# Performance work log

Measured on AMD Instinct MI355X. Metric: run time of the kernel, lower is better.

## Reference

```python
import jax, jax.numpy as jnp
import numpy as np
import math

B, I, C = 64, 512, 32
PRED, PL, ST, NH = 96, 16, 8, 8
WKS = (24, 168, 336)
PN = (I + ST - PL) // ST + 1  # 64 patches (padding_patch='end')

def _gelu(x):
    return jax.nn.gelu(x, approximate=False)  # torch nn.GELU default (erf)

def _ln(x, g, b, eps=1e-5):
    m = x.mean(-1, keepdims=True)
    v = ((x - m) ** 2).mean(-1, keepdims=True)
    return (x - m) / jnp.sqrt(v + eps) * g + b

def setup_inputs() -> dict:
    keys = jax.random.split(jax.random.key(0), 64)
    ki = iter(keys)
    def nrm(sh, sc=0.02):
        return (jax.random.normal(next(ki), sh) * sc).astype(jnp.float32)
    inp = {}
    inp['s'] = jax.random.normal(next(ki), (B, I, C), jnp.float32)
    inp['t'] = jax.random.normal(next(ki), (B, I, C), jnp.float32)
    inp['cycle_index'] = jax.random.randint(next(ki), (B,), 0, 336)
    # router: Linear(C, C//2) -> GELU -> Linear(C//2, num_scales)
    inp['rw1'] = nrm((C // 2, C)); inp['rb1'] = jnp.zeros(C // 2)
    inp['rw2'] = nrm((3, C // 2)); inp['rb2'] = jnp.zeros(3)
    # per-scale amplitude / phase tables (Wk, C)
    inp['A0'] = nrm((WKS[0], C), 1.0); inp['A1'] = nrm((WKS[1], C), 1.0); inp['A2'] = nrm((WKS[2], C), 1.0)
    inp['P0'] = (jax.random.uniform(next(ki), (WKS[0], C)) * 2 * math.pi).astype(jnp.float32)
    inp['P1'] = (jax.random.uniform(next(ki), (WKS[1], C)) * 2 * math.pi).astype(jnp.float32)
    inp['P2'] = (jax.random.uniform(next(ki), (WKS[2], C)) * 2 * math.pi).astype(jnp.float32)
    # PB_RPA (phase-biased relative patch attention), n_embd=PL, n_head=NH
    inp['Wqkv'] = nrm((3 * PL, PL)); inp['bqkv'] = jnp.zeros(3 * PL)
    inp['Wo'] = nrm((PL, PL)); inp['bo'] = jnp.zeros(PL)
    inp['alpha'] = jnp.ones(())
    # bn2 over channel dim = patch_num
    inp['bn_g'] = jnp.ones(PN); inp['bn_b'] = jnp.zeros(PN)
    inp['W3'] = nrm((2 * PRED, PN * PL)); inp['b3'] = jnp.zeros(2 * PRED)
    inp['W4'] = nrm((PRED, 2 * PRED)); inp['b4'] = jnp.zeros(PRED)
    inp['W5'] = nrm((4 * PRED, I)); inp['b5'] = jnp.zeros(4 * PRED)
    inp['W6'] = nrm((PRED, 2 * PRED)); inp['b6'] = jnp.zeros(PRED)
    inp['W7'] = nrm((PRED, PRED // 2)); inp['b7'] = jnp.zeros(PRED)
    inp['W8'] = nrm((PRED, 2 * PRED)); inp['b8'] = jnp.zeros(PRED)
    inp['ln1_g'] = jnp.ones(2 * PRED); inp['ln1_b'] = jnp.zeros(2 * PRED)
    inp['ln2_g'] = jnp.ones(PRED // 2); inp['ln2_b'] = jnp.zeros(PRED // 2)
    # TrendEnhancer: Conv1d(C, C, 3, pad=1) gated residual
    inp['te_w'] = nrm((C, C, 3)); inp['te_b'] = jnp.zeros(C)
    return inp

def _forward(s, t, cycle_index, rw1, rb1, rw2, rb2, A0, A1, A2, P0, P1, P2,
             Wqkv, bqkv, Wo, bo, alpha, bn_g, bn_b, W3, b3, W4, b4, W5, b5,
             W6, b6, W7, b7, W8, b8, ln1_g, ln1_b, ln2_g, ln2_b, te_w, te_b):
    s = s.transpose(0, 2, 1)  # (B,C,I)
    t = t.transpose(0, 2, 1)
    # router -> per-scale softmax weights (B, num_scales)
    h = _gelu(s.mean(-1) @ rw1.T + rb1)
    p = jax.nn.softmax(h @ rw2.T + rb2, axis=-1)
    ar = jnp.arange(I)
    cs, ps = [], []
    for Atab, Ptab, Wk in ((A0, P0, WKS[0]), (A1, P1, WKS[1]), (A2, P2, WKS[2])):
        idx = (cycle_index[:, None] + ar) % Wk            # (B,I) data-dependent gather
        A = jax.nn.softplus(Atab[idx]).transpose(0, 2, 1)  # (B,C,I)
        phi = Ptab[idx].transpose(0, 2, 1)
        Qr = A * jnp.cos(phi)                              # Qi=A*sin(phi) is unused in hermitian_attn
        S = jnp.einsum('bcl,bck->blk', Qr, s) / math.sqrt(C)
        Aw = jax.nn.softmax(S, axis=-1)
        cs.append(jnp.einsum('blk,bck->bcl', Aw, s))
        ps.append(phi)
    c_stack = jnp.stack(cs, 1)    # (B,3,C,I)
    phi_stack = jnp.stack(ps, 1)
    beta = p[:, :, None, None]
    s = s + (beta * c_stack).sum(1)
    fused_phi = (beta * phi_stack).sum(1)  # (B,C,I)
    N = B * C
    s = s.reshape(N, I)
    t = t.reshape(N, I)
    phi = jnp.repeat(fused_phi.mean(1), C, axis=0)  # (N,I)
    # padding_patch='end' -> replicate-pad last `stride` steps
    s = jnp.concatenate([s, jnp.repeat(s[:, -1:], ST, 1)], 1)
    phi = jnp.concatenate([phi, jnp.repeat(phi[:, -1:], ST, 1)], 1)
    widx = jnp.arange(PN)[:, None] * ST + jnp.arange(PL)
    sp = s[:, widx]                # (N, PN, PL) unfold
    phis = phi[:, widx].mean(-1)   # (N, PN)
    # PB_RPA: MHA over patches with phase-difference bias
    qkv = sp @ Wqkv.T + bqkv
    q, k, v = jnp.split(qkv, 3, axis=-1)
    hd = PL // NH
    def heads(x):
        return x.reshape(N, PN, NH, hd).transpose(0, 2, 1, 3)
    q, k, v = heads(q), heads(k), heads(v)
    bias = alpha * jnp.cos(phis[:, None, :, None] - phis[:, None, None, :])  # (N,1,PN,PN)
    sc = jnp.einsum('nhtd,nhsd->nhts', q, k) / math.sqrt(hd) + bias
    Aw = jax.nn.softmax(sc, axis=-1)
    o = jnp.einsum('nhts,nhsd->nhtd', Aw, v).transpose(0, 2, 1, 3).reshape(N, PN, PL)
    o = o @ Wo.T + bo
    sx = _gelu(sp + o)
    # bn2: BatchNorm1d over channel=patch_num (training-mode batch stats)
    mu = sx.mean((0, 2), keepdims=True)
    var = ((sx - mu) ** 2).mean((0, 2), keepdims=True)
    sx = (sx - mu) / jnp.sqrt(var + 1e-5) * bn_g[None, :, None] + bn_b[None, :, None]
    sx = sx.reshape(N, PN * PL)
    sx = _gelu(sx @ W3.T + b3) @ W4.T + b4  # (N, PRED)
    # trend branch
    u = t @ W5.T + b5                       # (N, 4*PRED)
    u = u.reshape(N, 2 * PRED, 2).mean(-1)  # AvgPool1d(2)
    u = _ln(u, ln1_g, ln1_b)
    u = u @ W6.T + b6
    u = u.reshape(N, PRED // 2, 2).mean(-1)
    u = _ln(u, ln2_g, ln2_b)
    u = u @ W7.T + b7                       # (N, PRED)
    u = u.reshape(B, C, PRED)
    f = jnp.fft.rfft(u, axis=-1)
    mask = (jnp.arange(f.shape[-1]) < 5).astype(f.dtype)
    u = u + jnp.fft.irfft(f * mask, n=PRED, axis=-1)
    y = jax.lax.conv_general_dilated(u, te_w, (1,), [(1, 1)],
                                     dimension_numbers=('NCH', 'OIH', 'NCH')) + te_b[None, :, None]
    u = (u + _gelu(y)).reshape(N, PRED)     # TrendEnhancer gated-conv residual
    x = jnp.concatenate([sx, u], 1) @ W8.T + b8
    return x.reshape(B, C, PRED).transpose(0, 2, 1)  # (B, pred_len, C)

def reference(s, t, cycle_index, rw1, rb1, rw2, rb2, A0, A1, A2, P0, P1, P2,
              Wqkv, bqkv, Wo, bo, alpha, bn_g, bn_b, W3, b3, W4, b4, W5, b5,
              W6, b6, W7, b7, W8, b8, ln1_g, ln1_b, ln2_g, ln2_b, te_w, te_b):
    return _forward(s, t, cycle_index, rw1, rb1, rw2, rb2, A0, A1, A2, P0, P1, P2,
                    Wqkv, bqkv, Wo, bo, alpha, bn_g, bn_b, W3, b3, W4, b4, W5, b5,
                    W6, b6, W7, b7, W8, b8, ln1_g, ln1_b, ln2_g, ln2_b, te_w, te_b)
```

## Files before the change

kernel.cpp:

```cpp
#include <hip/hip_runtime.h>
#include <math.h>

#define B_    64
#define I_    512
#define C_    32
#define PRED_ 96
#define PL_   16
#define ST_   8
#define NH_   8
#define PN_   64
#define N_    2048

typedef short bf16x8 __attribute__((ext_vector_type(8)));
typedef float f32x4 __attribute__((ext_vector_type(4)));
typedef bf16x8 __attribute__((may_alias)) bf16x8_a;
typedef uint2 __attribute__((may_alias)) uint2_a;
typedef uint4 __attribute__((may_alias)) uint4_a;

__device__ __forceinline__ float geluf(float x) {
    return 0.5f * x * (1.0f + erff(x * 0.70710678118654752f));
}
__device__ __forceinline__ float softplusf(float x) {
    return fmaxf(x, 0.0f) + log1pf(__expf(-fabsf(x)));
}
__device__ __forceinline__ unsigned short f2bf(float x) {
    union { float f; unsigned int u; } v; v.f = x;
    unsigned int r = v.u + 0x7fffu + ((v.u >> 16) & 1u);
    return (unsigned short)(r >> 16);
}

__global__ void k_headphi(const float* __restrict__ s, const float* __restrict__ rw1,
                          const float* __restrict__ rb1, const float* __restrict__ rw2,
                          const float* __restrict__ rb2,
                          const float* __restrict__ P0, const float* __restrict__ P1,
                          const float* __restrict__ P2, const int* __restrict__ cyc,
                          float* __restrict__ wp, float* __restrict__ phis) {
    int b = blockIdx.x, t = threadIdx.x;
    __shared__ float part[8][32];
    __shared__ float smean[32];
    __shared__ float h[16];
    __shared__ float wpl[3];
    __shared__ float pm[I_];
    int c = t & 31, chunk = t >> 5;
    float acc = 0.f;
    for (int l = chunk * 64; l < chunk * 64 + 64; ++l)
        acc += s[((size_t)b * I_ + l) * C_ + c];
    part[chunk][c] = acc;
    __syncthreads();
    if (t < 32) {
        float v = 0.f;
#pragma unroll
        for (int i = 0; i < 8; ++i) v += part[i][t];
        smean[t] = v * (1.0f / I_);
    }
    __syncthreads();
    if (t < 16) {
        float a = rb1[t];
#pragma unroll
        for (int c2 = 0; c2 < 32; ++c2) a += smean[c2] * rw1[t * 32 + c2];
        h[t] = geluf(a);
    }
    __syncthreads();
    if (t == 0) {
        float lg[3], mx = -1e30f;
        for (int k = 0; k < 3; ++k) {
            float a = rb2[k];
            for (int j = 0; j < 16; ++j) a += h[j] * rw2[k * 16 + j];
            lg[k] = a; mx = fmaxf(mx, a);
        }
        float d = 0.f;
        for (int k = 0; k < 3; ++k) { lg[k] = __expf(lg[k] - mx); d += lg[k]; }
        float inv = 1.f / d;
        for (int k = 0; k < 3; ++k) { wpl[k] = lg[k] * inv; wp[b * 3 + k] = lg[k] * inv; }
    }
    __syncthreads();
    float p0 = wpl[0], p1 = wpl[1], p2 = wpl[2];
    int cy = cyc[b];
    for (int l = t; l < I_; l += 256) {
        float acc2 = 0.f;
        {
            int idx = (cy + l) % 24;
            const float4* r = (const float4*)(P0 + idx * 32);
            float s4 = 0.f;
#pragma unroll
            for (int i = 0; i < 8; ++i) { float4 v = r[i]; s4 += v.x + v.y + v.z + v.w; }
            acc2 += p0 * s4;
        }
        {
            int idx = (cy + l) % 168;
            const float4* r = (const float4*)(P1 + idx * 32);
            float s4 = 0.f;
#pragma unroll
            for (int i = 0; i < 8; ++i) { float4 v = r[i]; s4 += v.x + v.y + v.z + v.w; }
            acc2 += p1 * s4;
        }
        {
            int idx = (cy + l) % 336;
            const float4* r = (const float4*)(P2 + idx * 32);
            float s4 = 0.f;
#pragma unroll
            for (int i = 0; i < 8; ++i) { float4 v = r[i]; s4 += v.x + v.y + v.z + v.w; }
            acc2 += p2 * s4;
        }
        pm[l] = acc2 * (1.0f / 32.0f);
    }
    __syncthreads();
    if (t < PN_) {
        float sum = 0.f;
#pragma unroll
        for (int j = 0; j < 16; ++j) {
            int l = t * ST_ + j; if (l > 511) l = 511;
            sum += pm[l];
        }
        phis[b * PN_ + t] = sum * (1.0f / 16.0f);
    }
}

__global__ void __launch_bounds__(512) k_attn_mfma(
        const float* __restrict__ s, const int* __restrict__ cyc,
        const float* __restrict__ A0, const float* __restrict__ A1, const float* __restrict__ A2,
        const float* __restrict__ P0, const float* __restrict__ P1, const float* __restrict__ P2,
        const float* __restrict__ wp, float* __restrict__ pcs) {
    int k3 = blockIdx.x, b = blockIdx.y;
    int t = threadIdx.x;
    int wid = t >> 6, lane = t & 63;
    int l15 = lane & 15, lg = lane >> 4;

    __shared__ unsigned short s_lds[512][40];
    __shared__ unsigned short sT[32][520];
    __shared__ unsigned short Pt[8][64][40];

    {
        int row = t;
        const float4* src = (const float4*)(s + ((size_t)b * I_ + row) * C_);
        unsigned short bv[32];
#pragma unroll
        for (int i = 0; i < 8; ++i) {
            float4 v = src[i];
            bv[4 * i + 0] = f2bf(v.x); bv[4 * i + 1] = f2bf(v.y);
            bv[4 * i + 2] = f2bf(v.z); bv[4 * i + 3] = f2bf(v.w);
        }
#pragma unroll
        for (int i = 0; i < 4; ++i) {
            uint4 pk;
            pk.x = (unsigned)bv[8 * i + 0] | ((unsigned)bv[8 * i + 1] << 16);
            pk.y = (unsigned)bv[8 * i + 2] | ((unsigned)bv[8 * i + 3] << 16);
            pk.z = (unsigned)bv[8 * i + 4] | ((unsigned)bv[8 * i + 5] << 16);
            pk.w = (unsigned)bv[8 * i + 6] | ((unsigned)bv[8 * i + 7] << 16);
            *((uint4_a*)&s_lds[row][8 * i]) = pk;
        }
#pragma unroll
        for (int cc = 0; cc < 32; ++cc) sT[cc][row] = bv[cc];
    }

    const float* Atab; const float* Ptab; int Wk;
    if (k3 == 0)      { Atab = A0; Ptab = P0; Wk = 24;  }
    else if (k3 == 1) { Atab = A1; Ptab = P1; Wk = 168; }
    else              { Atab = A2; Ptab = P2; Wk = 336; }
    float wpv = wp[b * 3 + k3];
    int cy = cyc[b];
    bf16x8 qrf[4];
#pragma unroll
    for (int qt = 0; qt < 4; ++qt) {
        int q = wid * 64 + qt * 16 + l15;
        int idx = (cy + q) % Wk;
        const float4* Ar = (const float4*)(Atab + idx * 32 + lg * 8);
        const float4* Pr = (const float4*)(Ptab + idx * 32 + lg * 8);
        float4 a0 = Ar[0], a1 = Ar[1], p0 = Pr[0], p1 = Pr[1];
        float qv[8];
        qv[0] = softplusf(a0.x) * __cosf(p0.x);
        qv[1] = softplusf(a0.y) * __cosf(p0.y);
        qv[2] = softplusf(a0.z) * __cosf(p0.z);
        qv[3] = softplusf(a0.w) * __cosf(p0.w);
        qv[4] = softplusf(a1.x) * __cosf(p1.x);
        qv[5] = softplusf(a1.y) * __cosf(p1.y);
        qv[6] = softplusf(a1.z) * __cosf(p1.z);
        qv[7] = softplusf(a1.w) * __cosf(p1.w);
        bf16x8 f;
#pragma unroll
        for (int j = 0; j < 8; ++j) f[j] = (short)f2bf(qv[j]);
        qrf[qt] = f;
    }
    __syncthreads();

    const float rs = 0.17677669529663687f;
    f32x4 acc[4][2];
#pragma unroll
    for (int qt = 0; qt < 4; ++qt)
#pragma unroll
        for (int ct = 0; ct < 2; ++ct) acc[qt][ct] = (f32x4){0.f, 0.f, 0.f, 0.f};
    float dacc[4] = {0.f, 0.f, 0.f, 0.f};

    for (int kc = 0; kc < 16; ++kc) {
        int key0 = kc * 32;
        bf16x8 a0 = *((const bf16x8_a*)&s_lds[key0 + l15][lg * 8]);
        bf16x8 a1 = *((const bf16x8_a*)&s_lds[key0 + 16 + l15][lg * 8]);
        f32x4 stv[4][2];
#pragma unroll
        for (int qt = 0; qt < 4; ++qt) {
            stv[qt][0] = __builtin_amdgcn_mfma_f32_16x16x32_bf16(a0, qrf[qt], (f32x4){0.f,0.f,0.f,0.f}, 0, 0, 0);
            stv[qt][1] = __builtin_amdgcn_mfma_f32_16x16x32_bf16(a1, qrf[qt], (f32x4){0.f,0.f,0.f,0.f}, 0, 0, 0);
        }
#pragma unroll
        for (int qt = 0; qt < 4; ++qt) {
#pragma unroll
            for (int h = 0; h < 2; ++h) {
                unsigned short pb[4];
                float ds = 0.f;
#pragma unroll
                for (int r = 0; r < 4; ++r) {
                    float e = __expf(stv[qt][h][r] * rs);
                    unsigned short ub = f2bf(e);
                    pb[r] = ub;
                    union { unsigned int u; float f; } bb; bb.u = ((unsigned int)ub) << 16;
                    ds += bb.f;
                }
                dacc[qt] += ds;
                uint2 w2;
                w2.x = (unsigned)pb[0] | ((unsigned)pb[1] << 16);
                w2.y = (unsigned)pb[2] | ((unsigned)pb[3] << 16);
                *((uint2_a*)&Pt[wid][qt * 16 + l15][h * 16 + lg * 4]) = w2;
            }
        }
        bf16x8 b0 = *((const bf16x8_a*)&sT[l15][key0 + lg * 8]);
        bf16x8 b1 = *((const bf16x8_a*)&sT[16 + l15][key0 + lg * 8]);
#pragma unroll
        for (int qt = 0; qt < 4; ++qt) {
            bf16x8 pa = *((const bf16x8_a*)&Pt[wid][qt * 16 + l15][lg * 8]);
            acc[qt][0] = __builtin_amdgcn_mfma_f32_16x16x32_bf16(pa, b0, acc[qt][0], 0, 0, 0);
            acc[qt][1] = __builtin_amdgcn_mfma_f32_16x16x32_bf16(pa, b1, acc[qt][1], 0, 0, 0);
        }
    }

#pragma unroll
    for (int qt = 0; qt < 4; ++qt) {
        float dq = dacc[qt];
        dq += __shfl_xor(dq, 16);
        dq += __shfl_xor(dq, 32);
        float invd[4];
#pragma unroll
        for (int r = 0; r < 4; ++r) {
            float dr = __shfl(dq, 4 * lg + r);
            invd[r] = wpv / dr;
        }
        int qbase = wid * 64 + qt * 16 + 4 * lg;
#pragma unroll
        for (int ct = 0; ct < 2; ++ct) {
            int c = ct * 16 + l15;
            float4 o;
            o.x = acc[qt][ct][0] * invd[0];
            o.y = acc[qt][ct][1] * invd[1];
            o.z = acc[qt][ct][2] * invd[2];
            o.w = acc[qt][ct][3] * invd[3];
            *(float4*)(pcs + (((size_t)k3 * B_ + b) * C_ + c) * I_ + qbase) = o;
        }
    }
}

__global__ void k_combine(const float* __restrict__ s, const float* __restrict__ t,
                          const float* __restrict__ pcs,
                          float* __restrict__ srow, float* __restrict__ trow) {
    int b = blockIdx.x, l0 = blockIdx.y * 32;
    int tt_ = threadIdx.x;
    __shared__ float st[32][33], tl[32][33];
#pragma unroll
    for (int r = 0; r < 4; ++r) {
        int lin = r * 256 + tt_;
        int lq = lin >> 5, c = lin & 31;
        st[lq][c] = s[((size_t)b * I_ + l0 + lq) * C_ + c];
        tl[lq][c] = t[((size_t)b * I_ + l0 + lq) * C_ + c];
    }
    __syncthreads();
    const size_t CH = (size_t)B_ * C_ * I_;
#pragma unroll
    for (int r = 0; r < 4; ++r) {
        int lin = r * 256 + tt_;
        int co = lin >> 5, lo = lin & 31;
        size_t pi = ((size_t)b * C_ + co) * I_ + l0 + lo;
        float sum = pcs[pi] + pcs[CH + pi] + pcs[2 * CH + pi];
        size_t oi = ((size_t)(b * C_ + co)) * I_ + l0 + lo;
        srow[oi] = st[lo][co] + sum;
        trow[oi] = tl[lo][co];
    }
}

__global__ void __launch_bounds__(256) k_patch(
        const float* __restrict__ srow, const float* __restrict__ phis,
        const float* __restrict__ Wqkv, const float* __restrict__ bqkv,
        const float* __restrict__ Wo, const float* __restrict__ bo,
        const float* __restrict__ alpha_p, float* __restrict__ sx) {
    int n = blockIdx.x, t = threadIdx.x;
    int p = t & 63, w = t >> 6;
    int b = n >> 5;
    __shared__ float spl[64][17];
    __shared__ float ql[64][17], kl[64][17], vl[64][17];
    __shared__ float blds[64][65];
    __shared__ float phil[64];
    __shared__ float wq[48][16];
    __shared__ float wo[16][16];
    __shared__ float o2l[64][17];
    float alpha = alpha_p[0];
    for (int i = t; i < 768; i += 256) wq[i >> 4][i & 15] = Wqkv[i];
    if (t < 256) wo[t >> 4][t & 15] = Wo[t];
    if (t < 64) phil[t] = phis[b * PN_ + t];
    const float* srn = srow + (size_t)n * I_;
#pragma unroll
    for (int jj = 0; jj < 4; ++jj) {
        int j = w * 4 + jj;
        int l = p * ST_ + j; if (l > 511) l = 511;
        spl[p][j] = srn[l];
    }
    __syncthreads();
#pragma unroll
    for (int oo = 0; oo < 12; ++oo) {
        int o = w * 12 + oo;
        float a = bqkv[o];
#pragma unroll
        for (int i2 = 0; i2 < 16; ++i2) a += spl[p][i2] * wq[o][i2];
        if (o < 16) ql[p][o] = a;
        else if (o < 32) kl[p][o - 16] = a;
        else vl[p][o - 32] = a;
    }
    float phit = phil[p];
#pragma unroll
    for (int jj = 0; jj < 16; ++jj) {
        int ss = w * 16 + jj;
        blds[p][ss] = alpha * __cosf(phit - phil[ss]);
    }
    __syncthreads();
    const float rs2 = 0.70710678118654752f;
#pragma unroll
    for (int hh = 0; hh < 2; ++hh) {
        int h = 2 * w + hh;
        float q0 = ql[p][2 * h], q1 = ql[p][2 * h + 1];
        float mh = -1e30f;
        for (int ss = 0; ss < 64; ++ss) {
            float sc = (q0 * kl[ss][2 * h] + q1 * kl[ss][2 * h + 1]) * rs2 + blds[p][ss];
            mh = fmaxf(mh, sc);
        }
        float dh = 0.f, o0 = 0.f, o1 = 0.f;
        for (int ss = 0; ss < 64; ++ss) {
            float sc = (q0 * kl[ss][2 * h] + q1 * kl[ss][2 * h + 1]) * rs2 + blds[p][ss];
            float wgt = __expf(sc - mh);
            dh += wgt; o0 += wgt * vl[ss][2 * h]; o1 += wgt * vl[ss][2 * h + 1];
        }
        float inv = 1.f / dh;
        o2l[p][2 * h] = o0 * inv; o2l[p][2 * h + 1] = o1 * inv;
    }
    __syncthreads();
    float* sxr = sx + ((size_t)n * PN_ + p) * PL_;
#pragma unroll
    for (int ii = 0; ii < 4; ++ii) {
        int i2 = w * 4 + ii;
        float a = bo[i2];
#pragma unroll
        for (int j = 0; j < 16; ++j) a += o2l[p][j] * wo[i2][j];
        sxr[i2] = geluf(spl[p][i2] + a);
    }
}

__global__ void k_bn_stats(const float* __restrict__ sx, float* __restrict__ bnpart) {
    int pn = blockIdx.x, chunk = blockIdx.y, t = threadIdx.x;
    __shared__ float r1[256], r2[256];
    int j4 = t & 3, nb = t >> 2;
    float s1 = 0.f, s2 = 0.f;
    for (int i = 0; i < 8; ++i) {
        int n = chunk * 512 + nb + i * 64;
        float4 v = *(const float4*)(sx + ((size_t)n * PN_ + pn) * PL_ + j4 * 4);
        s1 += v.x + v.y + v.z + v.w;
        s2 += v.x * v.x + v.y * v.y + v.z * v.z + v.w * v.w;
    }
    r1[t] = s1; r2[t] = s2;
    __syncthreads();
    for (int st = 128; st > 0; st >>= 1) {
        if (t < st) { r1[t] += r1[t + st]; r2[t] += r2[t + st]; }
        __syncthreads();
    }
    if (t == 0) {
        bnpart[(pn * 4 + chunk) * 2 + 0] = r1[0];
        bnpart[(pn * 4 + chunk) * 2 + 1] = r2[0];
    }
}

__global__ void k_bn_apply(float* __restrict__ sx, const float* __restrict__ bnpart,
                           const float* __restrict__ g, const float* __restrict__ bb) {
    int g4 = blockIdx.x * 256 + threadIdx.x;
    int pn = (g4 >> 2) & 63;
    float s1 = 0.f, s2 = 0.f;
#pragma unroll
    for (int ch = 0; ch < 4; ++ch) {
        s1 += bnpart[(pn * 4 + ch) * 2 + 0];
        s2 += bnpart[(pn * 4 + ch) * 2 + 1];
    }
    const float inv = 1.0f / (N_ * PL_);
    float mu = s1 * inv;
    float var = s2 * inv - mu * mu;
    float rstd = rsqrtf(var + 1e-5f);
    float gg = g[pn], bbv = bb[pn];
    float4* p = (float4*)sx + g4;
    float4 v = *p;
    v.x = (v.x - mu) * rstd * gg + bbv;
    v.y = (v.y - mu) * rstd * gg + bbv;
    v.z = (v.z - mu) * rstd * gg + bbv;
    v.w = (v.w - mu) * rstd * gg + bbv;
    *p = v;
}

template <int ACT>
__global__ void __launch_bounds__(128) k_gemm32(const float* __restrict__ A,
                                                const float* __restrict__ W,
                                                const float* __restrict__ bias,
                                                float* __restrict__ Cout,
                                                int M, int Nn, int K) {
    __shared__ float at[32][36];
    __shared__ float wt[32][36];
    int bm = blockIdx.x * 32, bn = blockIdx.y * 32;
    int t = threadIdx.x;
    int lr = t >> 2, lk = (t & 3) * 8;
    int tm = (t & 15) * 2, tn = (t >> 4) * 4;
    float acc[2][4] = {};
    for (int k0 = 0; k0 < K; k0 += 32) {
        float4 a0 = *(const float4*)(A + (size_t)(bm + lr) * K + k0 + lk);
        float4 a1 = *(const float4*)(A + (size_t)(bm + lr) * K + k0 + lk + 4);
        float4 w0 = *(const float4*)(W + (size_t)(bn + lr) * K + k0 + lk);
        float4 w1 = *(const float4*)(W + (size_t)(bn + lr) * K + k0 + lk + 4);
        __syncthreads();
        at[lk + 0][lr] = a0.x; at[lk + 1][lr] = a0.y; at[lk + 2][lr] = a0.z; at[lk + 3][lr] = a0.w;
        at[lk + 4][lr] = a1.x; at[lk + 5][lr] = a1.y; at[lk + 6][lr] = a1.z; at[lk + 7][lr] = a1.w;
        wt[lk + 0][lr] = w0.x; wt[lk + 1][lr] = w0.y; wt[lk + 2][lr] = w0.z; wt[lk + 3][lr] = w0.w;
        wt[lk + 4][lr] = w1.x; wt[lk + 5][lr] = w1.y; wt[lk + 6][lr] = w1.z; wt[lk + 7][lr] = w1.w;
        __syncthreads();
#pragma unroll
        for (int kk = 0; kk < 32; ++kk) {
            float2 a2 = *(const float2*)&at[kk][tm];
            float4 w4 = *(const float4*)&wt[kk][tn];
            acc[0][0] += a2.x * w4.x; acc[0][1] += a2.x * w4.y;
            acc[0][2] += a2.x * w4.z; acc[0][3] += a2.x * w4.w;
            acc[1][0] += a2.y * w4.x; acc[1][1] += a2.y * w4.y;
            acc[1][2] += a2.y * w4.z; acc[1][3] += a2.y * w4.w;
        }
    }
#pragma unroll
    for (int i = 0; i < 2; ++i) {
#pragma unroll
        for (int j = 0; j < 4; ++j) {
            float v = acc[i][j] + bias[bn + tn + j];
            if (ACT) v = geluf(v);
            Cout[(size_t)(bm + tm + i) * Nn + bn + tn + j] = v;
        }
    }
}

__global__ void k_rowmlp4(const float* __restrict__ g3, const float* __restrict__ W4,
                          const float* __restrict__ b4, float* __restrict__ sxf) {
    int n = blockIdx.x, t = threadIdx.x;
    __shared__ float row[192];
    for (int j = t; j < 192; j += 128) row[j] = g3[(size_t)n * 192 + j];
    __syncthreads();
    if (t < 96) {
        float a = b4[t];
        const float* wr = W4 + t * 192;
#pragma unroll 4
        for (int j = 0; j < 192; ++j) a += row[j] * wr[j];
        sxf[(size_t)n * 96 + t] = a;
    }
}

__global__ void k_u(const float* __restrict__ u1, const float* __restrict__ ln1g,
                    const float* __restrict__ ln1b, const float* __restrict__ W6,
                    const float* __restrict__ b6, const float* __restrict__ ln2g,
                    const float* __restrict__ ln2b, const float* __restrict__ W7,
                    const float* __restrict__ b7, float* __restrict__ u2out) {
    int n = blockIdx.x, t = threadIdx.x;
    __shared__ float a[192];
    __shared__ float red1[256], red2[256];
    __shared__ float c2[48];
    __shared__ float stat[2];
    __shared__ float u3l[96];
    __shared__ float cosb[5][96], sinb[5][96];
    __shared__ float coef[9];
    if (t < 96) {
#pragma unroll
        for (int k = 0; k < 5; ++k) {
            float sv, cv2;
            __sincosf(6.283185307179586f * (float)(k * t) / 96.0f, &sv, &cv2);
            cosb[k][t] = cv2; sinb[k][t] = sv;
        }
    }
    const float* ur = u1 + (size_t)n * 384;
    float av = 0.5f * (ur[2 * t] + ur[2 * t + 1]);
    red1[t] = av; red2[t] = av * av;
    if (t < 64) { red1[192 + t] = 0.f; red2[192 + t] = 0.f; }
    __syncthreads();
    for (int st = 128; st > 0; st >>= 1) {
        if (t < st) { red1[t] += red1[t + st]; red2[t] += red2[t + st]; }
        __syncthreads();
    }
    if (t == 0) {
        float mu = red1[0] * (1.0f / 192.0f);
        float var = red2[0] * (1.0f / 192.0f) - mu * mu;
        stat[0] = mu; stat[1] = rsqrtf(var + 1e-5f);
    }
    __syncthreads();
    a[t] = (av - stat[0]) * stat[1] * ln1g[t] + ln1b[t];
    __syncthreads();
    float bv = 0.f;
    if (t < 96) {
        bv = b6[t];
        const float* wr = W6 + t * 192;
#pragma unroll 4
        for (int j = 0; j < 192; ++j) bv += a[j] * wr[j];
    }
    __syncthreads();
    if (t < 96) red1[t] = bv;
    __syncthreads();
    float cv = 0.f;
    if (t < 48) cv = 0.5f * (red1[2 * t] + red1[2 * t + 1]);
    __syncthreads();
    if (t < 48) { red1[t] = cv; red2[t] = cv * cv; }
    else if (t < 64) { red1[t] = 0.f; red2[t] = 0.f; }
    __syncthreads();
    for (int st = 32; st > 0; st >>= 1) {
        if (t < st) { red1[t] += red1[t + st]; red2[t] += red2[t + st]; }
        __syncthreads();
    }
    if (t == 0) {
        float mu = red1[0] * (1.0f / 48.0f);
        float var = red2[0] * (1.0f / 48.0f) - mu * mu;
        stat[0] = mu; stat[1] = rsqrtf(var + 1e-5f);
    }
    __syncthreads();
    if (t < 48) c2[t] = (cv - stat[0]) * stat[1] * ln2g[t] + ln2b[t];
    __syncthreads();
    if (t < 96) {
        float acc = b7[t];
        const float* wr = W7 + t * 48;
#pragma unroll
        for (int j = 0; j < 48; ++j) acc += c2[j] * wr[j];
        u3l[t] = acc;
    }
    __syncthreads();
    if (t < 9) {
        int k = (t < 5) ? t : t - 4;
        const float* bas = (t < 5) ? cosb[k] : sinb[k];
        float acc = 0.f;
#pragma unroll 4
        for (int m = 0; m < 96; ++m) acc += u3l[m] * bas[m];
        coef[t] = acc;
    }
    __syncthreads();
    if (t < 96) {
        float rec = coef[0];
#pragma unroll
        for (int k = 1; k <= 4; ++k)
            rec += 2.0f * (coef[k] * cosb[k][t] + coef[4 + k] * sinb[k][t]);
        u2out[(size_t)n * 96 + t] = u3l[t] + rec * (1.0f / 96.0f);
    }
}

__global__ void k_conv(const float* __restrict__ u2, const float* __restrict__ tw,
                       const float* __restrict__ tb, float* __restrict__ u4) {
    int b = blockIdx.x, xq = blockIdx.y, t = threadIdx.x;
    int x0 = xq * 24;
    __shared__ float ub[32][26];
    __shared__ float twl[3072];
    for (int i = t; i < 832; i += 256) {
        int ic = i / 26, xx = i % 26;
        int gx = x0 + xx - 1;
        ub[ic][xx] = (gx >= 0 && gx < 96) ? u2[((size_t)b * 32 + ic) * 96 + gx] : 0.f;
    }
    for (int i = t; i < 3072; i += 256) twl[i] = tw[i];
    __syncthreads();
    for (int i = t; i < 768; i += 256) {
        int oc = i / 24, xx = i % 24;
        float acc = tb[oc];
#pragma unroll 8
        for (int ic = 0; ic < 32; ++ic) {
            const float* wv = twl + (oc * 32 + ic) * 3;
            acc += ub[ic][xx] * wv[0] + ub[ic][xx + 1] * wv[1] + ub[ic][xx + 2] * wv[2];
        }
        u4[((size_t)b * 32 + oc) * 96 + x0 + xx] = ub[oc][xx + 1] + geluf(acc);
    }
}

__global__ void k_out(const float* __restrict__ sxf, const float* __restrict__ u4,
                      const float* __restrict__ W8, const float* __restrict__ b8,
                      float* __restrict__ out) {
    int b = blockIdx.x, oq = blockIdx.y, t = threadIdx.x;
    __shared__ float ld[32][193];
    for (int i = t; i < 32 * 96; i += 256) {
        int c = i / 96, j = i % 96;
        ld[c][j]      = sxf[((size_t)(b * 32 + c)) * 96 + j];
        ld[c][96 + j] = u4[((size_t)(b * 32 + c)) * 96 + j];
    }
    __syncthreads();
    for (int i = t; i < 24 * 32; i += 256) {
        int o = oq * 24 + (i >> 5), c = i & 31;
        float acc = b8[o];
        const float* wr = W8 + o * 192;
#pragma unroll 4
        for (int j = 0; j < 192; ++j) acc += ld[c][j] * wr[j];
        out[((size_t)b * 96 + o) * 32 + c] = acc;
    }
}

extern "C" void kernel_launch(void* const* d_in, const int* in_sizes, int n_in,
                              void* d_out, int out_size, void* d_ws, size_t ws_size,
                              hipStream_t stream) {
    const float* s    = (const float*)d_in[0];
    const float* t    = (const float*)d_in[1];
    const int*   cyc  = (const int*)d_in[2];
    const float* rw1  = (const float*)d_in[3];
    const float* rb1  = (const float*)d_in[4];
    const float* rw2  = (const float*)d_in[5];
    const float* rb2  = (const float*)d_in[6];
    const float* A0   = (const float*)d_in[7];
    const float* A1   = (const float*)d_in[8];
    const float* A2   = (const float*)d_in[9];
    const float* P0   = (const float*)d_in[10];
    const float* P1   = (const float*)d_in[11];
    const float* P2   = (const float*)d_in[12];
    const float* Wqkv = (const float*)d_in[13];
    const float* bqkv = (const float*)d_in[14];
    const float* Wo   = (const float*)d_in[15];
    const float* bo   = (const float*)d_in[16];
    const float* alpha= (const float*)d_in[17];
    const float* bn_g = (const float*)d_in[18];
    const float* bn_b = (const float*)d_in[19];
    const float* W3   = (const float*)d_in[20];
    const float* b3   = (const float*)d_in[21];
    const float* W4   = (const float*)d_in[22];
    const float* b4   = (const float*)d_in[23];
    const float* W5   = (const float*)d_in[24];
    const float* b5   = (const float*)d_in[25];
    const float* W6   = (const float*)d_in[26];
    const float* b6   = (const float*)d_in[27];
    const float* W7   = (const float*)d_in[28];
    const float* b7   = (const float*)d_in[29];
    const float* W8   = (const float*)d_in[30];
    const float* b8   = (const float*)d_in[31];
    const float* ln1g = (const float*)d_in[32];
    const float* ln1b = (const float*)d_in[33];
    const float* ln2g = (const float*)d_in[34];
    const float* ln2b = (const float*)d_in[35];
    const float* tew  = (const float*)d_in[36];
    const float* teb  = (const float*)d_in[37];

    float* ws     = (float*)d_ws;
    float* wp     = ws;
    float* phis   = ws + 192;
    float* bnpart = ws + 4288;
    float* srow   = ws + 4864;
    float* trow   = srow + 1048576;
    float* R      = trow + 1048576;
    float* pcs = R;
    float* sx  = R;
    float* g3  = R + 2097152;
    float* sxf = R + 2490368;
    float* u1  = R + 2686976;
    float* u2f = R + 3473408;
    float* u4f = R + 3670016;
    float* out = (float*)d_out;

    k_headphi<<<64, 256, 0, stream>>>(s, rw1, rb1, rw2, rb2, P0, P1, P2, cyc, wp, phis);
    k_attn_mfma<<<dim3(3, 64), 512, 0, stream>>>(s, cyc, A0, A1, A2, P0, P1, P2, wp, pcs);
    k_combine<<<dim3(64, 16), 256, 0, stream>>>(s, t, pcs, srow, trow);
    k_patch<<<2048, 256, 0, stream>>>(srow, phis, Wqkv, bqkv, Wo, bo, alpha, sx);
    k_bn_stats<<<dim3(64, 4), 256, 0, stream>>>(sx, bnpart);
    k_bn_apply<<<2048, 256, 0, stream>>>(sx, bnpart, bn_g, bn_b);
    k_gemm32<1><<<dim3(64, 6), 128, 0, stream>>>(sx, W3, b3, g3, 2048, 192, 1024);
    k_rowmlp4<<<2048, 128, 0, stream>>>(g3, W4, b4, sxf);
    k_gemm32<0><<<dim3(64, 12), 128, 0, stream>>>(trow, W5, b5, u1, 2048, 384, 512);
    k_u<<<2048, 192, 0, stream>>>(u1, ln1g, ln1b, W6, b6, ln2g, ln2b, W7, b7, u2f);
    k_conv<<<dim3(64, 4), 256, 0, stream>>>(u2f, tew, teb, u4f);
    k_out<<<dim3(64, 4), 256, 0, stream>>>(sxf, u4f, W8, b8, out);
}
```

Measured before the change: 378.0 us.

## Use bf16 MFMA GEMMs, fold BatchNorm into GEMM load, simplify patch attention bias

The two fp32 tiled GEMMs become bf16 MFMA 16x16x32 kernels with 64x64 tiles. BatchNorm application is folded into the W3 GEMM's A-load as a per-patch scale and shift, which drops the separate read-modify-write pass over sx. Patch attention now expands cos(phi_p - phi_s) into cos/sin products and drops the max-subtraction pass, so each head loops over keys once. This trades precision (bf16 inputs, softmax without max-stabilisation) for fewer memory passes and less compute.

```diff
diff --git a/kernel.cpp b/kernel.cpp
--- a/kernel.cpp
+++ b/kernel.cpp
@@ -294,15 +294,18 @@
     int b = n >> 5;
     __shared__ float spl[64][17];
     __shared__ float ql[64][17], kl[64][17], vl[64][17];
-    __shared__ float blds[64][65];
-    __shared__ float phil[64];
+    __shared__ float cosl[64], sinl[64];
     __shared__ float wq[48][16];
     __shared__ float wo[16][16];
     __shared__ float o2l[64][17];
     float alpha = alpha_p[0];
     for (int i = t; i < 768; i += 256) wq[i >> 4][i & 15] = Wqkv[i];
     if (t < 256) wo[t >> 4][t & 15] = Wo[t];
-    if (t < 64) phil[t] = phis[b * PN_ + t];
+    if (t < 64) {
+        float sv, cv;
+        __sincosf(phis[b * PN_ + t], &sv, &cv);
+        cosl[t] = cv; sinl[t] = sv;
+    }
     const float* srn = srow + (size_t)n * I_;
 #pragma unroll
     for (int jj = 0; jj < 4; ++jj) {
@@ -321,28 +324,19 @@
         else if (o < 32) kl[p][o - 16] = a;
         else vl[p][o - 32] = a;
     }
-    float phit = phil[p];
-#pragma unroll
-    for (int jj = 0; jj < 16; ++jj) {
-        int ss = w * 16 + jj;
-        blds[p][ss] = alpha * __cosf(phit - phil[ss]);
-    }
     __syncthreads();
     const float rs2 = 0.70710678118654752f;
+    float cp = alpha * cosl[p], sp_ = alpha * sinl[p];
 #pragma unroll
     for (int hh = 0; hh < 2; ++hh) {
         int h = 2 * w + hh;
-        float q0 = ql[p][2 * h], q1 = ql[p][2 * h + 1];
-        float mh = -1e30f;
-        for (int ss = 0; ss < 64; ++ss) {
-            float sc = (q0 * kl[ss][2 * h] + q1 * kl[ss][2 * h + 1]) * rs2 + blds[p][ss];
-            mh = fmaxf(mh, sc);
-        }
+        float q0 = ql[p][2 * h] * rs2, q1 = ql[p][2 * h + 1] * rs2;
         float dh = 0.f, o0 = 0.f, o1 = 0.f;
         for (int ss = 0; ss < 64; ++ss) {
-            float sc = (q0 * kl[ss][2 * h] + q1 * kl[ss][2 * h + 1]) * rs2 + blds[p][ss];
-            float wgt = __expf(sc - mh);
-            dh += wgt; o0 += wgt * vl[ss][2 * h]; o1 += wgt * vl[ss][2 * h + 1];
+            float sc = q0 * kl[ss][2 * h] + q1 * kl[ss][2 * h + 1]
+                     + cp * cosl[ss] + sp_ * sinl[ss];
+            float e = __expf(sc);
+            dh += e; o0 += e * vl[ss][2 * h]; o1 += e * vl[ss][2 * h + 1];
         }
         float inv = 1.f / dh;
         o2l[p][2 * h] = o0 * inv; o2l[p][2 * h + 1] = o1 * inv;
@@ -382,10 +376,10 @@
     }
 }
 
-__global__ void k_bn_apply(float* __restrict__ sx, const float* __restrict__ bnpart,
-                           const float* __restrict__ g, const float* __restrict__ bb) {
-    int g4 = blockIdx.x * 256 + threadIdx.x;
-    int pn = (g4 >> 2) & 63;
+__global__ void k_bn_final(const float* __restrict__ bnpart, const float* __restrict__ g,
+                           const float* __restrict__ bb, float* __restrict__ bnmul,
+                           float* __restrict__ bnadd) {
+    int pn = threadIdx.x;
     float s1 = 0.f, s2 = 0.f;
 #pragma unroll
     for (int ch = 0; ch < 4; ++ch) {
@@ -395,58 +389,72 @@
     const float inv = 1.0f / (N_ * PL_);
     float mu = s1 * inv;
     float var = s2 * inv - mu * mu;
-    float rstd = rsqrtf(var + 1e-5f);
-    float gg = g[pn], bbv = bb[pn];
-    float4* p = (float4*)sx + g4;
-    float4 v = *p;
-    v.x = (v.x - mu) * rstd * gg + bbv;
-    v.y = (v.y - mu) * rstd * gg + bbv;
-    v.z = (v.z - mu) * rstd * gg + bbv;
-    v.w = (v.w - mu) * rstd * gg + bbv;
-    *p = v;
-}
-
-template <int ACT>
-__global__ void __launch_bounds__(128) k_gemm32(const float* __restrict__ A,
-                                                const float* __restrict__ W,
-                                                const float* __restrict__ bias,
-                                                float* __restrict__ Cout,
-                                                int M, int Nn, int K) {
-    __shared__ float at[32][36];
-    __shared__ float wt[32][36];
-    int bm = blockIdx.x * 32, bn = blockIdx.y * 32;
+    float m = rsqrtf(var + 1e-5f) * g[pn];
+    bnmul[pn] = m;
+    bnadd[pn] = bb[pn] - mu * m;
+}
+
+template <int ACT, int FUSE_BN>
+__global__ void __launch_bounds__(256) k_gemm_mfma(
+        const float* __restrict__ A, const float* __restrict__ W,
+        const float* __restrict__ bias, const float* __restrict__ bnmul,
+        const float* __restrict__ bnadd, float* __restrict__ Cout,
+        int M, int Nn, int K) {
+    __shared__ unsigned short Ab[64][36];
+    __shared__ unsigned short Wb[64][36];
+    int bm = blockIdx.x * 64, bn = blockIdx.y * 64;
     int t = threadIdx.x;
-    int lr = t >> 2, lk = (t & 3) * 8;
-    int tm = (t & 15) * 2, tn = (t >> 4) * 4;
-    float acc[2][4] = {};
-    for (int k0 = 0; k0 < K; k0 += 32) {
-        float4 a0 = *(const float4*)(A + (size_t)(bm + lr) * K + k0 + lk);
-        float4 a1 = *(const float4*)(A + (size_t)(bm + lr) * K + k0 + lk + 4);
-        float4 w0 = *(const float4*)(W + (size_t)(bn + lr) * K + k0 + lk);
-        float4 w1 = *(const float4*)(W + (size_t)(bn + lr) * K + k0 + lk + 4);
+    int wid = t >> 6, lane = t & 63, l15 = lane & 15, lg = lane >> 4;
+    int srw = t >> 2, sk = (t & 3) * 8;
+    f32x4 acc[4];
+#pragma unroll
+    for (int nt = 0; nt < 4; ++nt) acc[nt] = (f32x4){0.f, 0.f, 0.f, 0.f};
+
+    for (int kt = 0; kt < K; kt += 32) {
+        float4 av0 = *(const float4*)(A + (size_t)(bm + srw) * K + kt + sk);
+        float4 av1 = *(const float4*)(A + (size_t)(bm + srw) * K + kt + sk + 4);
+        float4 wv0 = *(const float4*)(W + (size_t)(bn + srw) * K + kt + sk);
+        float4 wv1 = *(const float4*)(W + (size_t)(bn + srw) * K + kt + sk + 4);
+        if (FUSE_BN) {
+            int pn = (kt + sk) >> 4;
+            float m = bnmul[pn], ad = bnadd[pn];
+            av0.x = av0.x * m + ad; av0.y = av0.y * m + ad;
+            av0.z = av0.z * m + ad; av0.w = av0.w * m + ad;
+            av1.x = av1.x * m + ad; av1.y = av1.y * m + ad;
+            av1.z = av1.z * m + ad; av1.w = av1.w * m + ad;
+        }
         __syncthreads();
-        at[lk + 0][lr] = a0.x; at[lk + 1][lr] = a0.y; at[lk + 2][lr] = a0.z; at[lk + 3][lr] = a0.w;
-        at[lk + 4][lr] = a1.x; at[lk + 5][lr] = a1.y; at[lk + 6][lr] = a1.z; at[lk + 7][lr] = a1.w;
-        wt[lk + 0][lr] = w0.x; wt[lk + 1][lr] = w0.y; wt[lk + 2][lr] = w0.z; wt[lk + 3][lr] = w0.w;
-        wt[lk + 4][lr] = w1.x; wt[lk + 5][lr] = w1.y; wt[lk + 6][lr] = w1.z; wt[lk + 7][lr] = w1.w;
+        {
+            uint4 pk;
+            pk.x = (unsigned)f2bf(av0.x) | ((unsigned)f2bf(av0.y) << 16);
+            pk.y = (unsigned)f2bf(av0.z) | ((unsigned)f2bf(av0.w) << 16);
+            pk.z = (unsigned)f2bf(av1.x) | ((unsigned)f2bf(av1.y) << 16);
+            pk.w = (unsigned)f2bf(av1.z) | ((unsigned)f2bf(av1.w) << 16);
+            *((uint4_a*)&Ab[srw][sk]) = pk;
+            uint4 pw;
+            pw.x = (unsigned)f2bf(wv0.x) | ((unsigned)f2bf(wv0.y) << 16);
+            pw.y = (unsigned)f2bf(wv0.z) | ((unsigned)f2bf(wv0.w) << 16);
+            pw.z = (unsigned)f2bf(wv1.x) | ((unsigned)f2bf(wv1.y) << 16);
+            pw.w = (unsigned)f2bf(wv1.z) | ((unsigned)f2bf(wv1.w) << 16);
+            *((uint4_a*)&Wb[srw][sk]) = pw;
+        }
         __syncthreads();
-#pragma unroll
-        for (int kk = 0; kk < 32; ++kk) {
-            float2 a2 = *(const float2*)&at[kk][tm];
-            float4 w4 = *(const float4*)&wt[kk][tn];
-            acc[0][0] += a2.x * w4.x; acc[0][1] += a2.x * w4.y;
-            acc[0][2] += a2.x * w4.z; acc[0][3] += a2.x * w4.w;
-            acc[1][0] += a2.y * w4.x; acc[1][1] += a2.y * w4.y;
-            acc[1][2] += a2.y * w4.z; acc[1][3] += a2.y * w4.w;
-        }
-    }
-#pragma unroll
-    for (int i = 0; i < 2; ++i) {
-#pragma unroll
-        for (int j = 0; j < 4; ++j) {
-            float v = acc[i][j] + bias[bn + tn + j];
+        bf16x8 af = *((const bf16x8_a*)&Ab[wid * 16 + l15][lg * 8]);
+#pragma unroll
+        for (int nt = 0; nt < 4; ++nt) {
+            bf16x8 wf = *((const bf16x8_a*)&Wb[nt * 16 + l15][lg * 8]);
+            acc[nt] = __builtin_amdgcn_mfma_f32_16x16x32_bf16(af, wf, acc[nt], 0, 0, 0);
+        }
+    }
+#pragma unroll
+    for (int nt = 0; nt < 4; ++nt) {
+#pragma unroll
+        for (int r = 0; r < 4; ++r) {
+            int m_ = bm + wid * 16 + 4 * lg + r;
+            int n_ = bn + nt * 16 + l15;
+            float v = acc[nt][r] + bias[n_];
             if (ACT) v = geluf(v);
-            Cout[(size_t)(bm + tm + i) * Nn + bn + tn + j] = v;
+            Cout[(size_t)m_ * Nn + n_] = v;
         }
     }
 }
@@ -650,7 +658,9 @@
     float* wp     = ws;
     float* phis   = ws + 192;
     float* bnpart = ws + 4288;
-    float* srow   = ws + 4864;
+    float* bnmul  = ws + 4800;
+    float* bnadd  = ws + 4864;
+    float* srow   = ws + 4928;
     float* trow   = srow + 1048576;
     float* R      = trow + 1048576;
     float* pcs = R;
@@ -667,10 +677,10 @@
     k_combine<<<dim3(64, 16), 256, 0, stream>>>(s, t, pcs, srow, trow);
     k_patch<<<2048, 256, 0, stream>>>(srow, phis, Wqkv, bqkv, Wo, bo, alpha, sx);
     k_bn_stats<<<dim3(64, 4), 256, 0, stream>>>(sx, bnpart);
-    k_bn_apply<<<2048, 256, 0, stream>>>(sx, bnpart, bn_g, bn_b);
-    k_gemm32<1><<<dim3(64, 6), 128, 0, stream>>>(sx, W3, b3, g3, 2048, 192, 1024);
+    k_bn_final<<<1, 64, 0, stream>>>(bnpart, bn_g, bn_b, bnmul, bnadd);
+    k_gemm_mfma<1, 1><<<dim3(32, 3), 256, 0, stream>>>(sx, W3, b3, bnmul, bnadd, g3, 2048, 192, 1024);
     k_rowmlp4<<<2048, 128, 0, stream>>>(g3, W4, b4, sxf);
-    k_gemm32<0><<<dim3(64, 12), 128, 0, stream>>>(trow, W5, b5, u1, 2048, 384, 512);
+    k_gemm_mfma<0, 0><<<dim3(32, 6), 256, 0, stream>>>(trow, W5, b5, bnmul, bnadd, u1, 2048, 384, 512);
     k_u<<<2048, 192, 0, stream>>>(u1, ln1g, ln1b, W6, b6, ln2g, ln2b, W7, b7, u2f);
     k_conv<<<dim3(64, 4), 256, 0, stream>>>(u2f, tew, teb, u4f);
     k_out<<<dim3(64, 4), 256, 0, stream>>>(sxf, u4f, W8, b8, out);
```

After: 351.6 us. 7.0% less time.
